# Kernel tuning notes

Measured on AMD Instinct MI355X. Metric: run time of the kernel, lower is better.

The kernel has to match this reference:

```python
import jax, jax.numpy as jnp
import numpy as np
from jax import lax

B, N, NP, NS, CIN = 4, 8192, 2048, 32, 64
RADIUS = 0.1
CH = [CIN + 3, 64, 64, 128]  # mlp[0] += 3 because use_xyz=True
EPS = 1e-5


def _gather(x, idx):
    # x: [B, N, D], idx: [B, ...] int -> [B, ..., D]
    return jax.vmap(lambda a, i: a[i])(x, idx)


def _fps(xyz, npoint):
    # furthest point sampling, returns indices [B, npoint]
    b, n, _ = xyz.shape
    init_idx = jnp.zeros((b,), jnp.int32)
    dist0 = jnp.full((b, n), 1e10, xyz.dtype)

    def body(carry, _):
        dist, last = carry
        p = jnp.take_along_axis(xyz, last[:, None, None], axis=1)  # [B,1,3]
        d = jnp.sum((xyz - p) ** 2, axis=-1)                       # [B,N]
        dist = jnp.minimum(dist, d)
        nxt = jnp.argmax(dist, axis=-1).astype(jnp.int32)
        return (dist, nxt), nxt

    (_, _), rest = lax.scan(body, (dist0, init_idx), None, length=npoint - 1)
    return jnp.concatenate([init_idx[None, :], rest], axis=0).T    # [B, npoint]


def _ball_query(xyz, new_xyz, radius, nsample):
    # first `nsample` points within radius; pad with the first hit (0 if none)
    n = xyz.shape[1]
    d2 = jnp.sum((new_xyz[:, :, None, :] - xyz[:, None, :, :]) ** 2, axis=-1)  # [B,NP,N]
    score = jnp.where(d2 < radius * radius, jnp.arange(n, dtype=jnp.int32), n)
    neg_vals, _ = lax.top_k(-score, nsample)   # smallest indices first
    idx = -neg_vals                            # [B,NP,nsample]
    first = idx[..., :1]
    fill = jnp.where(first >= n, 0, first)
    return jnp.where(idx >= n, fill, idx)


def setup_inputs() -> dict:
    key = jax.random.key(0)
    ks = jax.random.split(key, 16)
    inp = {
        "xyz": jax.random.uniform(ks[0], (B, N, 3), jnp.float32),
        "features": jax.random.normal(ks[1], (B, CIN, N), jnp.float32),
    }
    for i in range(3):
        ci, co = CH[i], CH[i + 1]
        inp[f"W{i}"] = jax.random.normal(ks[2 + 4 * i], (co, ci), jnp.float32) / np.sqrt(ci)
        inp[f"b{i}"] = jnp.zeros((co,), jnp.float32)
        inp[f"g{i}"] = jnp.ones((co,), jnp.float32)
        inp[f"beta{i}"] = jnp.zeros((co,), jnp.float32)
    return inp


def _forward(xyz, features, params):
    fps_idx = _fps(xyz, NP)
    new_xyz = _gather(xyz, fps_idx)                                 # [B,NP,3]
    idx = _ball_query(xyz, new_xyz, RADIUS, NS)                     # [B,NP,NS]
    g_xyz = _gather(xyz, idx) - new_xyz[:, :, None, :]              # relative xyz
    g_feat = _gather(jnp.swapaxes(features, 1, 2), idx)             # [B,NP,NS,CIN]
    h = jnp.concatenate([g_xyz, g_feat], axis=-1)                   # [B,NP,NS,3+CIN]
    for (W, b, g, be) in params:
        h = jnp.einsum('bpsc,oc->bpso', h, W) + b                   # 1x1 conv
        mu = jnp.mean(h, axis=(0, 1, 2))
        var = jnp.var(h, axis=(0, 1, 2))
        h = (h - mu) * lax.rsqrt(var + EPS) * g + be                # BatchNorm2d (batch stats)
        h = jax.nn.relu(h)
    new_features = jnp.max(h, axis=2)                               # max-pool over nsample
    return new_xyz, jnp.swapaxes(new_features, 1, 2)                # [B,Cout,NP]


def reference(xyz, features, W0, b0, g0, beta0, W1, b1, g1, beta1, W2, b2, g2, beta2):
    params = ((W0, b0, g0, beta0), (W1, b1, g1, beta1), (W2, b2, g2, beta2))
    return _forward(xyz, features, params)
```

## Files before the change

### kernel.cpp

```cpp
#include <hip/hip_runtime.h>
#include <hip/hip_bf16.h>
#include <cstdint>

#define B_   4
#define N_   8192
#define NP_  2048
#define NS_  32
#define CIN_ 64
#define M_   (B_*NP_*NS_)
#define EPS_ 1e-5f
#define R2_  0.01f

typedef unsigned long long ull;
typedef float v2f __attribute__((ext_vector_type(2)));

__global__ __launch_bounds__(256) void transpose_kernel(const float* __restrict__ feat,
                                                        __hip_bfloat16* __restrict__ featT)
{
    __shared__ float tile[64][65];
    const int b  = blockIdx.y;
    const int j0 = blockIdx.x * 64;
    const int tx = threadIdx.x & 63, ty = threadIdx.x >> 6;
    for (int cc = ty; cc < 64; cc += 4)
        tile[tx][cc] = feat[((size_t)(b*CIN_ + cc))*N_ + j0 + tx];
    __syncthreads();
    for (int cc = ty; cc < 64; cc += 4)
        featT[((size_t)(b*N_ + j0 + cc))*64 + tx] = __float2bfloat16(tile[cc][tx]);
}

template<int CTRL>
__device__ __forceinline__ float dppmaxf(float v)
{
    int o = __builtin_amdgcn_update_dpp(__float_as_int(v), __float_as_int(v), CTRL, 0xF, 0xF, false);
    return fmaxf(v, __int_as_float(o));
}

__global__ __launch_bounds__(512) void fps_kernel(const float* __restrict__ xyz,
    float* __restrict__ new_xyzf, float* __restrict__ out)
{
#pragma clang fp contract(off)
    const int b = blockIdx.x;
    const int t = threadIdx.x;
    const float* X = xyz + (size_t)b * N_ * 3;

    __shared__ float4 xyz4[N_];
    __shared__ unsigned short widxs[NP_];
    __shared__ ull slot;

    for (int p = t; p < N_; p += 512)
        xyz4[p] = make_float4(X[p*3+0], X[p*3+1], X[p*3+2], 0.f);
    if (t == 0) { slot = 0ull; widxs[0] = 0; }

    v2f px[8], py[8], pz[8], dst[8];
#pragma unroll
    for (int g = 0; g < 8; ++g) {
        const int p0 = (2*g)*512 + t, p1 = (2*g+1)*512 + t;
        px[g] = (v2f){X[p0*3+0], X[p1*3+0]};
        py[g] = (v2f){X[p0*3+1], X[p1*3+1]};
        pz[g] = (v2f){X[p0*3+2], X[p1*3+2]};
        dst[g] = (v2f){1e10f, 1e10f};
    }
    float cx = X[0], cy = X[1], cz = X[2];
    __syncthreads();

    for (int it = 1; it < NP_; ++it) {
        float bestv = -1.0f;
        const v2f c0 = (v2f){cx, cx}, c1 = (v2f){cy, cy}, c2 = (v2f){cz, cz};
#pragma unroll
        for (int g = 0; g < 8; ++g) {
            v2f dx = px[g] - c0, dy = py[g] - c1, dz = pz[g] - c2;
            v2f dd = dx*dx;
            dd = dd + dy*dy;
            dd = dd + dz*dz;
            v2f nd;
            nd.x = fminf(dst[g].x, dd.x);
            nd.y = fminf(dst[g].y, dd.y);
            dst[g] = nd;
            bestv = fmaxf(bestv, nd.x);
            bestv = fmaxf(bestv, nd.y);
        }
        float wm = bestv;
        wm = dppmaxf<0x111>(wm);
        wm = dppmaxf<0x112>(wm);
        wm = dppmaxf<0x114>(wm);
        wm = dppmaxf<0x118>(wm);
        wm = dppmaxf<0x142>(wm);
        wm = dppmaxf<0x143>(wm);
        const float wm_b = __int_as_float(__builtin_amdgcn_readlane(__float_as_int(wm), 63));
        if (bestv == wm_b) {
            int idx = 0;
#pragma unroll
            for (int g = 7; g >= 0; --g) {
                if (dst[g].y == wm_b) idx = (2*g+1)*512 + t;
                if (dst[g].x == wm_b) idx = (2*g)*512 + t;
            }
            const ull key = ((ull)(unsigned)it << 45)
                          | ((ull)__float_as_uint(wm_b) << 13)
                          | (ull)(unsigned)(8191 - idx);
            atomicMax(&slot, key);
        }
        __syncthreads();
        const ull k = slot;
        const int widx = 8191 - (int)(k & 0x1fffull);
        if (t == 0) widxs[it] = (unsigned short)widx;
        const float4 c = xyz4[widx];
        cx = c.x; cy = c.y; cz = c.z;
    }
    __syncthreads();
    for (int i = t; i < NP_; i += 512) {
        const float4 c = xyz4[widxs[i]];
        const size_t o3 = ((size_t)(b*NP_ + i)) * 3;
        new_xyzf[o3] = c.x; new_xyzf[o3+1] = c.y; new_xyzf[o3+2] = c.z;
        out[o3] = c.x; out[o3+1] = c.y; out[o3+2] = c.z;
    }
}

__global__ __launch_bounds__(256) void ball_kernel(const float* __restrict__ xyz,
    const float* __restrict__ new_xyzf, int* __restrict__ ballidx)
{
#pragma clang fp contract(off)
    const int gw   = (blockIdx.x * 256 + threadIdx.x) >> 6;
    const int lane = threadIdx.x & 63;
    const int b    = gw >> 11;
    const float* X = xyz + (size_t)b * N_ * 3;
    const float cx = new_xyzf[(size_t)gw*3];
    const float cy = new_xyzf[(size_t)gw*3+1];
    const float cz = new_xyzf[(size_t)gw*3+2];
    int* outp = ballidx + (size_t)gw * NS_;
    int total = 0, first = -1;
    for (int base = 0; base < N_; base += 64) {
        const int j = base + lane;
        float dx = cx - X[j*3], dy = cy - X[j*3+1], dz = cz - X[j*3+2];
        float d2 = dx*dx;
        d2 = d2 + dy*dy;
        d2 = d2 + dz*dz;
        const bool in = d2 <= R2_;
        ull m = __ballot(in);
        if (m) {
            if (first < 0) first = base + __builtin_ctzll(m);
            int r = total + __popcll(m & ((1ull << lane) - 1ull));
            if (in && r < NS_) outp[r] = j;
            total += (int)__popcll(m);
            if (total >= NS_) break;
        }
    }
    if (total < NS_) {
        int f = first < 0 ? 0 : first;
        if (lane >= total && lane < NS_) outp[lane] = f;
    }
}

__global__ __launch_bounds__(256) void gemm1_kernel(const float* __restrict__ xyz,
    const __hip_bfloat16* __restrict__ featT, const float* __restrict__ newxyz,
    const int* __restrict__ ballidx, const float* __restrict__ W, const float* __restrict__ bias,
    __hip_bfloat16* __restrict__ pre1, float* __restrict__ psum, float* __restrict__ psumsq)
{
    const int lane = threadIdx.x & 63;
    const int gw   = (blockIdx.x * 256 + threadIdx.x) >> 6;
    float w[67];
#pragma unroll
    for (int k = 0; k < 67; ++k) w[k] = W[lane*67 + k];
    const float bs = bias[lane];
    float s1 = 0.f, s2 = 0.f;
    for (int r = gw; r < M_; r += 4096) {
        const int b = r >> 16;
        const int p = (r & 65535) >> 5;
        const int j = ballidx[r];
        const float* xp = xyz    + ((size_t)b*N_  + j)*3;
        const float* cp = newxyz + ((size_t)b*NP_ + p)*3;
        float acc = bs;
        acc = fmaf(xp[0] - cp[0], w[0], acc);
        acc = fmaf(xp[1] - cp[1], w[1], acc);
        acc = fmaf(xp[2] - cp[2], w[2], acc);
        const uint4* rp = (const uint4*)(featT + ((size_t)b*N_ + j)*64);
#pragma unroll
        for (int q = 0; q < 8; ++q) {
            const uint4 u4 = rp[q];
            const unsigned uu0 = u4.x, uu1 = u4.y, uu2 = u4.z, uu3 = u4.w;
            acc = fmaf(__uint_as_float(uu0 << 16),         w[3 + q*8 + 0], acc);
            acc = fmaf(__uint_as_float(uu0 & 0xffff0000u), w[3 + q*8 + 1], acc);
            acc = fmaf(__uint_as_float(uu1 << 16),         w[3 + q*8 + 2], acc);
            acc = fmaf(__uint_as_float(uu1 & 0xffff0000u), w[3 + q*8 + 3], acc);
            acc = fmaf(__uint_as_float(uu2 << 16),         w[3 + q*8 + 4], acc);
            acc = fmaf(__uint_as_float(uu2 & 0xffff0000u), w[3 + q*8 + 5], acc);
            acc = fmaf(__uint_as_float(uu3 << 16),         w[3 + q*8 + 6], acc);
            acc = fmaf(__uint_as_float(uu3 & 0xffff0000u), w[3 + q*8 + 7], acc);
        }
        pre1[(size_t)r*64 + lane] = __float2bfloat16(acc);
        s1 += acc;
        s2 = fmaf(acc, acc, s2);
    }
    psum  [(size_t)gw*64 + lane] = s1;
    psumsq[(size_t)gw*64 + lane] = s2;
}

__global__ __launch_bounds__(256) void epi_kernel(__hip_bfloat16* __restrict__ buf,
    const float* __restrict__ sc, const float* __restrict__ sh)
{
    __shared__ float ssc[64], ssh[64];
    if (threadIdx.x < 64) { ssc[threadIdx.x] = sc[threadIdx.x]; ssh[threadIdx.x] = sh[threadIdx.x]; }
    __syncthreads();
    const size_t idx = (size_t)blockIdx.x * 256 + threadIdx.x;
    const int k0 = (threadIdx.x & 7) * 8;
    uint4* p = (uint4*)buf;
    uint4 u = p[idx];
    unsigned wds[4] = {u.x, u.y, u.z, u.w};
    unsigned res[4];
#pragma unroll
    for (int m = 0; m < 4; ++m) {
        const int k = k0 + m*2;
        float v0 = __uint_as_float(wds[m] << 16);
        float v1 = __uint_as_float(wds[m] & 0xffff0000u);
        v0 = fmaxf(fmaf(v0, ssc[k],   ssh[k]),   0.f);
        v1 = fmaxf(fmaf(v1, ssc[k+1], ssh[k+1]), 0.f);
        __hip_bfloat16 b0 = __float2bfloat16(v0);
        __hip_bfloat16 b1 = __float2bfloat16(v1);
        unsigned short s0 = *reinterpret_cast<unsigned short*>(&b0);
        unsigned short s1 = *reinterpret_cast<unsigned short*>(&b1);
        res[m] = (unsigned)s0 | ((unsigned)s1 << 16);
    }
    p[idx] = make_uint4(res[0], res[1], res[2], res[3]);
}

__global__ __launch_bounds__(256) void gemm2_kernel(__hip_bfloat16* __restrict__ buf,
    const float* __restrict__ W, const float* __restrict__ bias,
    float* __restrict__ psum, float* __restrict__ psumsq)
{
    const int lane = threadIdx.x & 63;
    const int gw   = (blockIdx.x * 256 + threadIdx.x) >> 6;
    float w[64];
#pragma unroll
    for (int k = 0; k < 64; ++k) w[k] = W[lane*64 + k];
    const float bs = bias[lane];
    float s1 = 0.f, s2 = 0.f;
    for (int r = gw; r < M_; r += 4096) {
        const uint4* rp = (const uint4*)(buf + (size_t)r*64);
        float acc = bs;
#pragma unroll
        for (int q = 0; q < 8; ++q) {
            const uint4 u4 = rp[q];
            const unsigned uu0 = u4.x, uu1 = u4.y, uu2 = u4.z, uu3 = u4.w;
            acc = fmaf(__uint_as_float(uu0 << 16),         w[q*8 + 0], acc);
            acc = fmaf(__uint_as_float(uu0 & 0xffff0000u), w[q*8 + 1], acc);
            acc = fmaf(__uint_as_float(uu1 << 16),         w[q*8 + 2], acc);
            acc = fmaf(__uint_as_float(uu1 & 0xffff0000u), w[q*8 + 3], acc);
            acc = fmaf(__uint_as_float(uu2 << 16),         w[q*8 + 4], acc);
            acc = fmaf(__uint_as_float(uu2 & 0xffff0000u), w[q*8 + 5], acc);
            acc = fmaf(__uint_as_float(uu3 << 16),         w[q*8 + 6], acc);
            acc = fmaf(__uint_as_float(uu3 & 0xffff0000u), w[q*8 + 7], acc);
        }
        buf[(size_t)r*64 + lane] = __float2bfloat16(acc);
        s1 += acc;
        s2 = fmaf(acc, acc, s2);
    }
    psum  [(size_t)gw*64 + lane] = s1;
    psumsq[(size_t)gw*64 + lane] = s2;
}

__global__ __launch_bounds__(256) void gemm3_kernel(const __hip_bfloat16* __restrict__ act2,
    const float* __restrict__ W, const float* __restrict__ bias,
    float* __restrict__ mxb, float* __restrict__ mnb,
    float* __restrict__ psum, float* __restrict__ psumsq)
{
    const int lane = threadIdx.x & 63;
    const int gw   = (blockIdx.x * 256 + threadIdx.x) >> 6;
    const int pt   = gw >> 1;
    const int half = gw & 1;
    const int o = half*64 + lane;
    float w[64];
#pragma unroll
    for (int k = 0; k < 64; ++k) w[k] = W[o*64 + k];
    const float bs = bias[o];
    float s1 = 0.f, s2 = 0.f, mx = -1e30f, mn = 1e30f;
    for (int s = 0; s < NS_; ++s) {
        const size_t r = (size_t)pt*NS_ + s;
        const uint4* rp = (const uint4*)(act2 + r*64);
        float acc = bs;
#pragma unroll
        for (int q = 0; q < 8; ++q) {
            const uint4 u4 = rp[q];
            const unsigned uu0 = u4.x, uu1 = u4.y, uu2 = u4.z, uu3 = u4.w;
            acc = fmaf(__uint_as_float(uu0 << 16),         w[q*8 + 0], acc);
            acc = fmaf(__uint_as_float(uu0 & 0xffff0000u), w[q*8 + 1], acc);
            acc = fmaf(__uint_as_float(uu1 << 16),         w[q*8 + 2], acc);
            acc = fmaf(__uint_as_float(uu1 & 0xffff0000u), w[q*8 + 3], acc);
            acc = fmaf(__uint_as_float(uu2 << 16),         w[q*8 + 4], acc);
            acc = fmaf(__uint_as_float(uu2 & 0xffff0000u), w[q*8 + 5], acc);
            acc = fmaf(__uint_as_float(uu3 << 16),         w[q*8 + 6], acc);
            acc = fmaf(__uint_as_float(uu3 & 0xffff0000u), w[q*8 + 7], acc);
        }
        s1 += acc;
        s2 = fmaf(acc, acc, s2);
        mx = fmaxf(mx, acc);
        mn = fminf(mn, acc);
    }
    mxb[(size_t)pt*128 + o] = mx;
    mnb[(size_t)pt*128 + o] = mn;
    psum  [(size_t)pt*128 + o] = s1;
    psumsq[(size_t)pt*128 + o] = s2;
}

template<int CO>
__global__ __launch_bounds__(256) void bnred_kernel(const float* __restrict__ psum,
    const float* __restrict__ psumsq, const float* __restrict__ g, const float* __restrict__ beta,
    float* __restrict__ sc, float* __restrict__ sh, int nslots)
{
    const int c = blockIdx.x;
    const int t = threadIdx.x;
    float s1 = 0, s2 = 0;
    for (int i = t; i < nslots; i += 256) {
        s1 += psum  [(size_t)i*CO + c];
        s2 += psumsq[(size_t)i*CO + c];
    }
    __shared__ float a1[256], a2[256];
    a1[t] = s1; a2[t] = s2;
    __syncthreads();
    for (int st = 128; st > 0; st >>= 1) {
        if (t < st) { a1[t] += a1[t+st]; a2[t] += a2[t+st]; }
        __syncthreads();
    }
    if (t == 0) {
        const float invM = 1.0f / (float)M_;
        float mu  = a1[0] * invM;
        float var = fmaxf(a2[0] * invM - mu*mu, 0.f);
        float rs  = 1.0f / sqrtf(var + EPS_);
        float s   = rs * g[c];
        sc[c] = s;
        sh[c] = fmaf(-mu, s, beta[c]);
    }
}

__global__ __launch_bounds__(256) void final_kernel(const float* __restrict__ mxb,
    const float* __restrict__ mnb, const float* __restrict__ sc, const float* __restrict__ sh,
    float* __restrict__ out)
{
    __shared__ float tile[128][65];
    const int b = blockIdx.y, p0 = blockIdx.x * 64;
    {
        const int o = threadIdx.x & 127, ph = threadIdx.x >> 7;
        const float s = sc[o], h = sh[o];
        const bool pos = (s >= 0.f);
        for (int pl = ph; pl < 64; pl += 2) {
            const size_t pt = (size_t)b*NP_ + p0 + pl;
            float v = pos ? mxb[pt*128 + o] : mnb[pt*128 + o];
            tile[o][pl] = fmaxf(fmaf(v, s, h), 0.f);
        }
    }
    __syncthreads();
    {
        const int p = threadIdx.x & 63, oh = threadIdx.x >> 6;
        for (int oo = oh; oo < 128; oo += 4)
            out[(size_t)(B_*NP_*3) + ((size_t)(b*128 + oo))*NP_ + p0 + p] = tile[oo][p];
    }
}

extern "C" void kernel_launch(void* const* d_in, const int* in_sizes, int n_in,
                              void* d_out, int out_size, void* d_ws, size_t ws_size,
                              hipStream_t stream)
{
    const float* xyz  = (const float*)d_in[0];
    const float* feat = (const float*)d_in[1];
    const float* W0   = (const float*)d_in[2];
    const float* b0   = (const float*)d_in[3];
    const float* g0   = (const float*)d_in[4];
    const float* be0  = (const float*)d_in[5];
    const float* W1   = (const float*)d_in[6];
    const float* b1   = (const float*)d_in[7];
    const float* g1   = (const float*)d_in[8];
    const float* be1  = (const float*)d_in[9];
    const float* W2   = (const float*)d_in[10];
    const float* b2   = (const float*)d_in[11];
    const float* g2   = (const float*)d_in[12];
    const float* be2  = (const float*)d_in[13];

    char* ws = (char*)d_ws;
    float* newxyz = (float*)(ws + 32768);
    int*   ball   = (int*)  (ws + 131072);
    float* scb    = (float*)(ws + 1179648);
    float* psum   = (float*)(ws + 1183744);
    float* psumsq = (float*)(ws + 5378048);
    __hip_bfloat16* featT = (__hip_bfloat16*)(ws + 9572352);
    float* mxb    = (float*)(ws + 13766656);
    float* mnb    = (float*)(ws + 17960960);
    __hip_bfloat16* buf1 = (__hip_bfloat16*)(ws + 22155264);
    float* out = (float*)d_out;

    float* sc1 = scb;       float* sh1 = scb + 128;
    float* sc2 = scb + 256; float* sh2 = scb + 384;
    float* sc3 = scb + 512; float* sh3 = scb + 640;

    transpose_kernel<<<dim3(N_/64, B_), 256, 0, stream>>>(feat, featT);
    fps_kernel<<<dim3(B_), 512, 0, stream>>>(xyz, newxyz, out);
    ball_kernel<<<dim3(B_*NP_/4), 256, 0, stream>>>(xyz, newxyz, ball);

    gemm1_kernel<<<1024, 256, 0, stream>>>(xyz, featT, newxyz, ball, W0, b0, buf1, psum, psumsq);
    bnred_kernel<64><<<64, 256, 0, stream>>>(psum, psumsq, g0, be0, sc1, sh1, 4096);
    epi_kernel<<<M_*64/8/256, 256, 0, stream>>>(buf1, sc1, sh1);
    gemm2_kernel<<<1024, 256, 0, stream>>>(buf1, W1, b1, psum, psumsq);
    bnred_kernel<64><<<64, 256, 0, stream>>>(psum, psumsq, g1, be1, sc2, sh2, 4096);
    epi_kernel<<<M_*64/8/256, 256, 0, stream>>>(buf1, sc2, sh2);
    gemm3_kernel<<<4096, 256, 0, stream>>>(buf1, W2, b2, mxb, mnb, psum, psumsq);
    bnred_kernel<128><<<128, 256, 0, stream>>>(psum, psumsq, g2, be2, sc3, sh3, 8192);
    final_kernel<<<dim3(NP_/64, B_), 256, 0, stream>>>(mxb, mnb, sc3, sh3, out);
}
```

Before: 2.597 ms.

## Fold feature transpose into FPS launch and rework per-iteration argmax reduction

The transpose kernel is merged into the FPS launch as extra blocks, so the transpose runs alongside the four long-running FPS blocks and one launch is removed. Inside FPS, the 64-bit iteration-tagged atomicMax is replaced by a per-wave max written to shared memory, a block-wide max read after a barrier, and a 32-bit atomicMax on the inverted index in a double-buffered slot. This adds a second barrier per iteration in exchange for a cheaper atomic and fewer contending lanes. The transpose blocks also share the FPS kernel's large static LDS allocation, which may limit how many can co-reside.

```diff
diff --git a/kernel.cpp b/kernel.cpp
--- a/kernel.cpp
+++ b/kernel.cpp
@@ -14,20 +14,6 @@
 typedef unsigned long long ull;
 typedef float v2f __attribute__((ext_vector_type(2)));
 
-__global__ __launch_bounds__(256) void transpose_kernel(const float* __restrict__ feat,
-                                                        __hip_bfloat16* __restrict__ featT)
-{
-    __shared__ float tile[64][65];
-    const int b  = blockIdx.y;
-    const int j0 = blockIdx.x * 64;
-    const int tx = threadIdx.x & 63, ty = threadIdx.x >> 6;
-    for (int cc = ty; cc < 64; cc += 4)
-        tile[tx][cc] = feat[((size_t)(b*CIN_ + cc))*N_ + j0 + tx];
-    __syncthreads();
-    for (int cc = ty; cc < 64; cc += 4)
-        featT[((size_t)(b*N_ + j0 + cc))*64 + tx] = __float2bfloat16(tile[cc][tx]);
-}
-
 template<int CTRL>
 __device__ __forceinline__ float dppmaxf(float v)
 {
@@ -36,20 +22,38 @@
 }
 
 __global__ __launch_bounds__(512) void fps_kernel(const float* __restrict__ xyz,
+    const float* __restrict__ feat, __hip_bfloat16* __restrict__ featT,
     float* __restrict__ new_xyzf, float* __restrict__ out)
 {
 #pragma clang fp contract(off)
-    const int b = blockIdx.x;
-    const int t = threadIdx.x;
-    const float* X = xyz + (size_t)b * N_ * 3;
-
     __shared__ float4 xyz4[N_];
     __shared__ unsigned short widxs[NP_];
-    __shared__ ull slot;
+    __shared__ float wavemax[8];
+    __shared__ unsigned widx_slot[2];
+    __shared__ float tile[64][65];
+
+    const int t = threadIdx.x;
+
+    if (blockIdx.x >= B_) {
+        const int blk = blockIdx.x - B_;
+        const int b   = blk >> 7;
+        const int j0  = (blk & 127) * 64;
+        const int tx = t & 63, ty = t >> 6;
+        for (int cc = ty; cc < 64; cc += 8)
+            tile[tx][cc] = feat[((size_t)(b*CIN_ + cc))*N_ + j0 + tx];
+        __syncthreads();
+        for (int cc = ty; cc < 64; cc += 8)
+            featT[((size_t)(b*N_ + j0 + cc))*64 + tx] = __float2bfloat16(tile[cc][tx]);
+        return;
+    }
+
+    const int b = blockIdx.x;
+    const float* X = xyz + (size_t)b * N_ * 3;
 
     for (int p = t; p < N_; p += 512)
         xyz4[p] = make_float4(X[p*3+0], X[p*3+1], X[p*3+2], 0.f);
-    if (t == 0) { slot = 0ull; widxs[0] = 0; }
+    if (t < 2) widx_slot[t] = 0u;
+    if (t == 0) widxs[0] = 0;
 
     v2f px[8], py[8], pz[8], dst[8];
 #pragma unroll
@@ -60,10 +64,11 @@
         pz[g] = (v2f){X[p0*3+2], X[p1*3+2]};
         dst[g] = (v2f){1e10f, 1e10f};
     }
+    const int wv = t >> 6, ln = t & 63;
     float cx = X[0], cy = X[1], cz = X[2];
-    __syncthreads();
 
     for (int it = 1; it < NP_; ++it) {
+        const int par = it & 1;
         float bestv = -1.0f;
         const v2f c0 = (v2f){cx, cx}, c1 = (v2f){cy, cy}, c2 = (v2f){cz, cz};
 #pragma unroll
@@ -86,22 +91,22 @@
         wm = dppmaxf<0x118>(wm);
         wm = dppmaxf<0x142>(wm);
         wm = dppmaxf<0x143>(wm);
-        const float wm_b = __int_as_float(__builtin_amdgcn_readlane(__float_as_int(wm), 63));
-        if (bestv == wm_b) {
-            int idx = 0;
+        if (ln == 63) wavemax[wv] = wm;
+        __syncthreads();
+        if (t == 0) widx_slot[par ^ 1] = 0u;
+        float bmax = fmaxf(fmaxf(fmaxf(wavemax[0], wavemax[1]), fmaxf(wavemax[2], wavemax[3])),
+                           fmaxf(fmaxf(wavemax[4], wavemax[5]), fmaxf(wavemax[6], wavemax[7])));
+        if (bestv == bmax) {
+            unsigned nin = 0u;
 #pragma unroll
             for (int g = 7; g >= 0; --g) {
-                if (dst[g].y == wm_b) idx = (2*g+1)*512 + t;
-                if (dst[g].x == wm_b) idx = (2*g)*512 + t;
+                if (dst[g].y == bmax) nin = ~(unsigned)((2*g+1)*512 + t);
+                if (dst[g].x == bmax) nin = ~(unsigned)((2*g)*512 + t);
             }
-            const ull key = ((ull)(unsigned)it << 45)
-                          | ((ull)__float_as_uint(wm_b) << 13)
-                          | (ull)(unsigned)(8191 - idx);
-            atomicMax(&slot, key);
+            atomicMax(&widx_slot[par], nin);
         }
         __syncthreads();
-        const ull k = slot;
-        const int widx = 8191 - (int)(k & 0x1fffull);
+        const int widx = (int)(~widx_slot[par]);
         if (t == 0) widxs[it] = (unsigned short)widx;
         const float4 c = xyz4[widx];
         cx = c.x; cy = c.y; cz = c.z;
@@ -389,8 +394,7 @@
     float* sc2 = scb + 256; float* sh2 = scb + 384;
     float* sc3 = scb + 512; float* sh3 = scb + 640;
 
-    transpose_kernel<<<dim3(N_/64, B_), 256, 0, stream>>>(feat, featT);
-    fps_kernel<<<dim3(B_), 512, 0, stream>>>(xyz, newxyz, out);
+    fps_kernel<<<dim3(B_ + B_*(N_/64)), 512, 0, stream>>>(xyz, feat, featT, newxyz, out);
     ball_kernel<<<dim3(B_*NP_/4), 256, 0, stream>>>(xyz, newxyz, ball);
 
     gemm1_kernel<<<1024, 256, 0, stream>>>(xyz, featT, newxyz, ball, W0, b0, buf1, psum, psumsq);
```

New measurement: 2.315 ms. 1.12x faster.
